# Kernel optimization log

Hardware: AMD Instinct MI355X
Metric: run time of the kernel (lower is better)

## Reference

```python
import jax, jax.numpy as jnp
import numpy as np

D_MODEL = 1024
NUM_HEADS = 16
HEAD_DIM = D_MODEL // NUM_HEADS


def setup_inputs() -> dict:
    key = jax.random.key(0)
    ks = jax.random.split(key, 5)
    scale = 1.0 / np.sqrt(D_MODEL)
    x = jax.random.normal(ks[0], (2, 2048, D_MODEL), dtype=jnp.float32)
    W_qkv = jax.random.normal(ks[1], (D_MODEL, 3 * D_MODEL), dtype=jnp.float32) * scale
    b_qkv = jnp.zeros((3 * D_MODEL,), dtype=jnp.float32)
    W_proj = jax.random.normal(ks[2], (D_MODEL, D_MODEL), dtype=jnp.float32) * scale
    b_proj = jnp.zeros((D_MODEL,), dtype=jnp.float32)
    return {"x": x, "W_qkv": W_qkv, "b_qkv": b_qkv, "W_proj": W_proj, "b_proj": b_proj}


def reference(x, W_qkv, b_qkv, W_proj, b_proj):
    B, S, D = x.shape
    qkv = x @ W_qkv + b_qkv                      # [B,S,3D]
    qkv = qkv.reshape(B, S, 3, NUM_HEADS, HEAD_DIM)
    qkv = jnp.transpose(qkv, (2, 0, 3, 1, 4))    # [3,B,H,S,hd]
    q, k, v = qkv[0], qkv[1], qkv[2]
    scores = jnp.einsum('bhqd,bhkd->bhqk', q, k) / jnp.sqrt(jnp.asarray(HEAD_DIM, x.dtype))
    probs = jax.nn.softmax(scores, axis=-1)
    out = jnp.einsum('bhqk,bhkd->bhqd', probs, v)  # [B,H,S,hd]
    out = jnp.transpose(out, (0, 2, 1, 3)).reshape(B, S, D)
    return out @ W_proj + b_proj
```

## Files before the change

### kernel.cpp

```cpp
#include <hip/hip_runtime.h>
#include <math.h>

#define B_ 2
#define S_ 2048
#define D_ 1024
#define H_ 16
#define HD_ 64

typedef __bf16 bf16x8 __attribute__((ext_vector_type(8)));
typedef __bf16 bf16x4 __attribute__((ext_vector_type(4)));
typedef __bf16 bf16x2 __attribute__((ext_vector_type(2)));
typedef float f32x4 __attribute__((ext_vector_type(4)));
typedef float f32x16 __attribute__((ext_vector_type(16)));
typedef unsigned u32x2 __attribute__((ext_vector_type(2)));

#define GLOAD16(gsrc, ldst) \
  __builtin_amdgcn_global_load_lds((const __attribute__((address_space(1))) void*)(gsrc), \
                                   (__attribute__((address_space(3))) void*)(ldst), 16, 0, 0)

#define QSCALE 0.18033688f

static __device__ __forceinline__ unsigned pack2(float a, float b) {
    bf16x2 v; v[0] = (__bf16)a; v[1] = (__bf16)b;
    return __builtin_bit_cast(unsigned, v);
}

__global__ __launch_bounds__(256) void prep_k(
    const float* __restrict__ x, __bf16* __restrict__ x_bf,
    const float* __restrict__ Wqkv, __bf16* __restrict__ wq_t,
    const float* __restrict__ Wproj, __bf16* __restrict__ wp_t)
{
    __shared__ float t[64][65];
    const int tid = threadIdx.x;
    const int bid = blockIdx.x;

    if (bid < 2048) {
        int i = (bid * 256 + tid) * 8;
        float4 a = *(const float4*)(x + i);
        float4 b = *(const float4*)(x + i + 4);
        bf16x8 v;
        v[0] = (__bf16)a.x; v[1] = (__bf16)a.y; v[2] = (__bf16)a.z; v[3] = (__bf16)a.w;
        v[4] = (__bf16)b.x; v[5] = (__bf16)b.y; v[6] = (__bf16)b.z; v[7] = (__bf16)b.w;
        *(bf16x8*)(x_bf + i) = v;
        return;
    }

    const float* in; __bf16* outp; int K, N, qcols; float qs; int bx, by;
    if (bid < 2816) {
        int tt = bid - 2048; bx = tt % 48; by = tt / 48;
        in = Wqkv; outp = wq_t; K = D_; N = 3 * D_; qcols = D_; qs = QSCALE;
    } else {
        int tt = bid - 2816; bx = tt % 16; by = tt / 16;
        in = Wproj; outp = wp_t; K = D_; N = D_; qcols = 0; qs = 1.0f;
    }
    const int bj = bx * 64;
    const int bi = by * 64;
    #pragma unroll
    for (int it = 0; it < 4; ++it) {
        int idx = (tid + it * 256) * 4;
        int r = idx >> 6, c = idx & 63;
        float4 v = *(const float4*)(in + (size_t)(bi + r) * N + bj + c);
        t[r][c] = v.x; t[r][c+1] = v.y; t[r][c+2] = v.z; t[r][c+3] = v.w;
    }
    __syncthreads();
    int j = tid & 63;
    int i0 = (tid >> 6) * 16;
    float s = (bj + j) < qcols ? qs : 1.0f;
    bf16x8 h0, h1;
    #pragma unroll
    for (int ii = 0; ii < 8; ++ii) h0[ii] = (__bf16)(t[i0 + ii][j] * s);
    #pragma unroll
    for (int ii = 0; ii < 8; ++ii) h1[ii] = (__bf16)(t[i0 + 8 + ii][j] * s);
    size_t o = (size_t)(bj + j) * K + bi + i0;
    *(bf16x8*)(outp + o) = h0; *(bf16x8*)(outp + o + 8) = h1;
}

template<typename OutT>
__global__ __launch_bounds__(256) void gemm_nt_k(
    const __bf16* __restrict__ A, const __bf16* __restrict__ Bt,
    const float* __restrict__ bias, OutT* __restrict__ C,
    int M, int N, int K, int qcols, float qs)
{
    constexpr int TSZ = 128 * 64;
    __shared__ __bf16 sA[TSZ];
    __shared__ __bf16 sB[TSZ];

    const int tid = threadIdx.x, w = tid >> 6, l = tid & 63;
    const int lr = l & 15, lg = l >> 4;
    const int bm = blockIdx.y * 128, bn = blockIdx.x * 128;
    const int wm = w >> 1, wn = w & 1;

    f32x4 acc[4][4] = {};

    for (int k0 = 0; k0 < K; k0 += 64) {
        __syncthreads();
        #pragma unroll
        for (int c = 0; c < 4; ++c) {
            int q = w * 4 + c;
            int r = q * 8 + (l >> 3);
            int sl = ((l & 7) ^ (r & 7)) * 8;
            GLOAD16(A + (size_t)(bm + r) * K + k0 + sl, sA + q * 512);
            GLOAD16(Bt + (size_t)(bn + r) * K + k0 + sl, sB + q * 512);
        }
        __syncthreads();
        #pragma unroll
        for (int kk = 0; kk < 2; ++kk) {
            bf16x8 ah[4], bh[4];
            #pragma unroll
            for (int i = 0; i < 4; ++i) {
                int ra = wm * 64 + i * 16 + lr;
                int sa = ((kk * 4 + lg) ^ (ra & 7)) * 8;
                ah[i] = *(const bf16x8*)(sA + ra * 64 + sa);
                int rb = wn * 64 + i * 16 + lr;
                int sb = ((kk * 4 + lg) ^ (rb & 7)) * 8;
                bh[i] = *(const bf16x8*)(sB + rb * 64 + sb);
            }
            #pragma unroll
            for (int mi = 0; mi < 4; ++mi)
                #pragma unroll
                for (int ni = 0; ni < 4; ++ni)
                    acc[mi][ni] = __builtin_amdgcn_mfma_f32_16x16x32_bf16(ah[mi], bh[ni], acc[mi][ni], 0, 0, 0);
        }
    }

    #pragma unroll
    for (int ni = 0; ni < 4; ++ni) {
        int col = bn + wn * 64 + ni * 16 + lr;
        float bv = bias[col];
        if (col < qcols) bv *= qs;
        #pragma unroll
        for (int mi = 0; mi < 4; ++mi) {
            #pragma unroll
            for (int r = 0; r < 4; ++r) {
                int row = bm + wm * 64 + mi * 16 + lg * 4 + r;
                float v = acc[mi][ni][r] + bv;
                C[(size_t)row * N + col] = (OutT)v;
            }
        }
    }
}

__global__ __launch_bounds__(512) void attn32_k(
    const __bf16* __restrict__ qkv, __bf16* __restrict__ Pout,
    float* __restrict__ Lout)
{
    __shared__ __bf16 Ks[2][2][64 * 64];
    __shared__ __bf16 Vt[2][2][64 * 64];

    const int tid = threadIdx.x, w = tid >> 6, l = tid & 63;
    const int q32 = l & 31, hi = l >> 5;
    const int bid = blockIdx.x;
    const int X = bid >> 5, hb = bid & 31;
    const int qt = X >> 1, kvh = X & 1;
    const int h = hb >> 1, b = hb & 1;
    const int q0 = qt * 256;
    const int kvbase = kvh * 1024;
    const size_t ldq = 3 * D_;
    const __bf16* Qg = qkv + (size_t)b * S_ * ldq + h * HD_;
    const __bf16* Kg = Qg + D_;
    const __bf16* Vg = Qg + 2 * D_;
    const int qg = q0 + w * 32 + q32;

    bf16x8 qf[4];
    #pragma unroll
    for (int ds = 0; ds < 4; ++ds)
        qf[ds] = *(const bf16x8*)(Qg + (size_t)qg * ldq + ds * 16 + hi * 8);

    const int krow = tid >> 3;
    const int ksl  = (tid & 7) ^ (krow & 7);
    const int vk   = tid & 63;
    const int vd0  = (tid >> 6) * 8;
    int voff[8];
    #pragma unroll
    for (int j = 0; j < 8; ++j)
        voff[j] = (vd0 + j) * 128 + (((vk >> 3) ^ j) * 16) + (vk & 7) * 2;

    f32x16 o[2] = {};
    float lsumA = 0.f, lsumB = 0.f;
    bf16x8 vrA, vrB;

    auto stageK = [&](int lt, int set, int t) {
        GLOAD16(Kg + (size_t)(kvbase + lt * 64 + krow) * ldq + ksl * 8,
                &Ks[set][t][w * 512]);
    };
    auto loadV = [&](int lt) {
        return *(const bf16x8*)(Vg + (size_t)(kvbase + lt * 64 + vk) * ldq + vd0);
    };
    auto writeV = [&](int set, int t, const bf16x8& vr) {
        #pragma unroll
        for (int j = 0; j < 8; ++j)
            *(__bf16*)((char*)&Vt[set][t][0] + voff[j]) = vr[j];
    };

    auto smPack = [&](f32x16 sc[2], bf16x8 pa[2][2], float& ls) {
        float sum = 0.f;
        #pragma unroll
        for (int kb = 0; kb < 2; ++kb)
            #pragma unroll
            for (int i = 0; i < 16; ++i) {
                float pv = __builtin_amdgcn_exp2f(sc[kb][i]);
                sc[kb][i] = pv;
                sum += pv;
            }
        ls += sum;
        #pragma unroll
        for (int kb = 0; kb < 2; ++kb)
            #pragma unroll
            for (int tl = 0; tl < 2; ++tl) {
                int base = tl * 8;
                unsigned A0 = pack2(sc[kb][base + 0], sc[kb][base + 1]);
                unsigned A1 = pack2(sc[kb][base + 2], sc[kb][base + 3]);
                unsigned B0 = pack2(sc[kb][base + 4], sc[kb][base + 5]);
                unsigned B1 = pack2(sc[kb][base + 6], sc[kb][base + 7]);
                u32x2 s0 = __builtin_amdgcn_permlane32_swap(A0, B0, false, false);
                u32x2 s1 = __builtin_amdgcn_permlane32_swap(A1, B1, false, false);
                union { unsigned u[4]; bf16x8 v; } pu;
                pu.u[0] = s0[0]; pu.u[1] = s1[0]; pu.u[2] = s0[1]; pu.u[3] = s1[1];
                pa[kb][tl] = pu.v;
            }
    };

    auto computePair = [&](int set) {
        f32x16 sc0[2] = {};
        __builtin_amdgcn_s_setprio(1);
        #pragma unroll
        for (int kb = 0; kb < 2; ++kb) {
            int r = kb * 32 + q32;
            #pragma unroll
            for (int ds = 0; ds < 4; ++ds) {
                int slot = (ds * 2 + hi) ^ (r & 7);
                bf16x8 kf = *(const bf16x8*)((const char*)&Ks[set][0][0] + r * 128 + slot * 16);
                sc0[kb] = __builtin_amdgcn_mfma_f32_32x32x16_bf16(kf, qf[ds], sc0[kb], 0, 0, 0);
            }
        }
        __builtin_amdgcn_s_setprio(0);

        bf16x8 pa0[2][2];
        smPack(sc0, pa0, lsumA);

        f32x16 sc1[2] = {};
        __builtin_amdgcn_s_setprio(1);
        #pragma unroll
        for (int st = 0; st < 4; ++st) {
            {
                int r = q32;
                int slot = (st * 2 + hi) ^ (r & 7);
                bf16x8 kf = *(const bf16x8*)((const char*)&Ks[set][1][0] + r * 128 + slot * 16);
                sc1[0] = __builtin_amdgcn_mfma_f32_32x32x16_bf16(kf, qf[st], sc1[0], 0, 0, 0);
            }
            {
                int dr = q32;
                int slot = (st * 2 + hi) ^ (dr & 7);
                bf16x8 vf = *(const bf16x8*)((const char*)&Vt[set][0][0] + dr * 128 + slot * 16);
                o[0] = __builtin_amdgcn_mfma_f32_32x32x16_bf16(vf, pa0[st >> 1][st & 1], o[0], 0, 0, 0);
            }
            {
                int r = 32 + q32;
                int slot = (st * 2 + hi) ^ (r & 7);
                bf16x8 kf = *(const bf16x8*)((const char*)&Ks[set][1][0] + r * 128 + slot * 16);
                sc1[1] = __builtin_amdgcn_mfma_f32_32x32x16_bf16(kf, qf[st], sc1[1], 0, 0, 0);
            }
            {
                int dr = 32 + q32;
                int slot = (st * 2 + hi) ^ (dr & 7);
                bf16x8 vf = *(const bf16x8*)((const char*)&Vt[set][0][0] + dr * 128 + slot * 16);
                o[1] = __builtin_amdgcn_mfma_f32_32x32x16_bf16(vf, pa0[st >> 1][st & 1], o[1], 0, 0, 0);
            }
        }
        __builtin_amdgcn_s_setprio(0);

        bf16x8 pa1[2][2];
        smPack(sc1, pa1, lsumB);

        __builtin_amdgcn_s_setprio(1);
        #pragma unroll
        for (int db = 0; db < 2; ++db) {
            int dr = db * 32 + q32;
            #pragma unroll
            for (int tt = 0; tt < 4; ++tt) {
                int slot = (tt * 2 + hi) ^ (dr & 7);
                bf16x8 vf = *(const bf16x8*)((const char*)&Vt[set][1][0] + dr * 128 + slot * 16);
                o[db] = __builtin_amdgcn_mfma_f32_32x32x16_bf16(vf, pa1[tt >> 1][tt & 1], o[db], 0, 0, 0);
            }
        }
        __builtin_amdgcn_s_setprio(0);
    };

    stageK(0, 0, 0); stageK(1, 0, 1);
    vrA = loadV(0);  vrB = loadV(1);
    writeV(0, 0, vrA); writeV(0, 1, vrB);
    __syncthreads();

    constexpr int NP = 8;
    for (int pr = 0; pr < NP; ++pr) {
        const int set = pr & 1, nset = set ^ 1;
        if (pr < NP - 1) {
            stageK(2 * pr + 2, nset, 0);
            stageK(2 * pr + 3, nset, 1);
            vrA = loadV(2 * pr + 2);
            vrB = loadV(2 * pr + 3);
        }
        computePair(set);
        if (pr < NP - 1) {
            writeV(nset, 0, vrA);
            writeV(nset, 1, vrB);
        }
        __syncthreads();
    }

    float lsum = lsumA + lsumB;
    lsum += __shfl_xor(lsum, 32);
    const size_t orow = (size_t)b * S_ + qg;
    __bf16* Pb = Pout + (size_t)kvh * (4096 * 1024) + orow * D_ + h * HD_;
    #pragma unroll
    for (int db = 0; db < 2; ++db)
        #pragma unroll
        for (int rg = 0; rg < 4; ++rg) {
            int d = db * 32 + 8 * rg + 4 * hi;
            bf16x4 ov;
            #pragma unroll
            for (int i = 0; i < 4; ++i) ov[i] = (__bf16)o[db][rg * 4 + i];
            *(bf16x4*)(Pb + d) = ov;
        }
    if (hi == 0)
        Lout[(size_t)kvh * (4096 * 16) + orow * 16 + h] = lsum;
}

__global__ __launch_bounds__(256) void combine_k(
    const __bf16* __restrict__ P, const float* __restrict__ L,
    __bf16* __restrict__ attnb)
{
    int i = (blockIdx.x * 256 + threadIdx.x) * 8;
    int row = i >> 10;
    int h = (i & 1023) >> 6;
    float l0 = L[row * 16 + h];
    float l1 = L[4096 * 16 + row * 16 + h];
    float inv = 1.0f / (l0 + l1);
    bf16x8 p0 = *(const bf16x8*)(P + i);
    bf16x8 p1 = *(const bf16x8*)(P + 4096 * 1024 + i);
    bf16x8 r;
    #pragma unroll
    for (int j = 0; j < 8; ++j)
        r[j] = (__bf16)(((float)p0[j] + (float)p1[j]) * inv);
    *(bf16x8*)(attnb + i) = r;
}

extern "C" void kernel_launch(void* const* d_in, const int* in_sizes, int n_in,
                              void* d_out, int out_size, void* d_ws, size_t ws_size,
                              hipStream_t stream) {
    const float* x     = (const float*)d_in[0];
    const float* Wqkv  = (const float*)d_in[1];
    const float* bqkv  = (const float*)d_in[2];
    const float* Wproj = (const float*)d_in[3];
    const float* bproj = (const float*)d_in[4];

    __bf16* ws = (__bf16*)d_ws;
    const size_t MB = 524288;
    __bf16* wp_t  = ws;
    __bf16* qkv   = ws + 2 * MB;
    __bf16* attnb = ws + 26 * MB;
    __bf16* x_bf  = ws + 34 * MB;
    __bf16* wq_t  = ws + 42 * MB;
    __bf16* Pp    = ws + 34 * MB;
    float*  Lp    = (float*)(ws + 50 * MB);

    const int M = B_ * S_;

    prep_k<<<3072, 256, 0, stream>>>(x, x_bf, Wqkv, wq_t, Wproj, wp_t);

    gemm_nt_k<__bf16><<<dim3(24, 32), 256, 0, stream>>>(
        x_bf, wq_t, bqkv, qkv, M, 3 * D_, D_, D_, QSCALE);

    attn32_k<<<512, 512, 0, stream>>>(qkv, Pp, Lp);

    combine_k<<<2048, 256, 0, stream>>>(Pp, Lp, attnb);

    gemm_nt_k<float><<<dim3(8, 32), 256, 0, stream>>>(
        attnb, wp_t, bproj, (float*)d_out, M, D_, D_, 0, 1.0f);
}
```

Measured before the change: 136.3 us.

## Restructure attention to 4 waves each owning 64 queries, sharing K/V fragments

The attention kernel now runs 4 waves of 256 threads instead of 8, and each wave handles two 32-query groups. Every K and V fragment read from LDS feeds two MFMAs, which halves the LDS reads per unit of math. The K/V tiles shrink to one 64-row tile per stage, double-buffered, and the loop runs over 16 single tiles instead of 8 pairs. This gives up the interleaved pair schedule, which overlapped QK^T of the second tile with PV of the first, and it roughly doubles accumulator and Q register use per wave, which could limit occupancy. Launch bounds ask for 2 blocks per CU.

```diff
diff --git a/kernel.cpp b/kernel.cpp
--- a/kernel.cpp
+++ b/kernel.cpp
@@ -140,12 +140,12 @@
     }
 }
 
-__global__ __launch_bounds__(512) void attn32_k(
+__global__ __launch_bounds__(256, 2) void attn32_k(
     const __bf16* __restrict__ qkv, __bf16* __restrict__ Pout,
     float* __restrict__ Lout)
 {
-    __shared__ __bf16 Ks[2][2][64 * 64];
-    __shared__ __bf16 Vt[2][2][64 * 64];
+    __shared__ __bf16 Ks[2][64 * 64];
+    __shared__ __bf16 Vt[2][64 * 64];
 
     const int tid = threadIdx.x, w = tid >> 6, l = tid & 63;
     const int q32 = l & 31, hi = l >> 5;
@@ -159,37 +159,49 @@
     const __bf16* Qg = qkv + (size_t)b * S_ * ldq + h * HD_;
     const __bf16* Kg = Qg + D_;
     const __bf16* Vg = Qg + 2 * D_;
-    const int qg = q0 + w * 32 + q32;
-
-    bf16x8 qf[4];
-    #pragma unroll
-    for (int ds = 0; ds < 4; ++ds)
-        qf[ds] = *(const bf16x8*)(Qg + (size_t)qg * ldq + ds * 16 + hi * 8);
-
-    const int krow = tid >> 3;
-    const int ksl  = (tid & 7) ^ (krow & 7);
-    const int vk   = tid & 63;
-    const int vd0  = (tid >> 6) * 8;
-    int voff[8];
-    #pragma unroll
-    for (int j = 0; j < 8; ++j)
-        voff[j] = (vd0 + j) * 128 + (((vk >> 3) ^ j) * 16) + (vk & 7) * 2;
-
-    f32x16 o[2] = {};
-    float lsumA = 0.f, lsumB = 0.f;
-    bf16x8 vrA, vrB;
-
-    auto stageK = [&](int lt, int set, int t) {
-        GLOAD16(Kg + (size_t)(kvbase + lt * 64 + krow) * ldq + ksl * 8,
-                &Ks[set][t][w * 512]);
+    const int qg0 = q0 + w * 64 + q32;
+
+    bf16x8 qf0[4], qf1[4];
+    #pragma unroll
+    for (int ds = 0; ds < 4; ++ds) {
+        qf0[ds] = *(const bf16x8*)(Qg + (size_t)qg0 * ldq + ds * 16 + hi * 8);
+        qf1[ds] = *(const bf16x8*)(Qg + (size_t)(qg0 + 32) * ldq + ds * 16 + hi * 8);
+    }
+
+    int krow[2], ksl[2], voff[2][8];
+    const int vk = l;
+    #pragma unroll
+    for (int c = 0; c < 2; ++c) {
+        int p = (w * 2 + c) * 64 + l;
+        krow[c] = p >> 3;
+        ksl[c]  = (p & 7) ^ (krow[c] & 7);
+        int d0 = (w * 2 + c) * 8;
+        #pragma unroll
+        for (int j = 0; j < 8; ++j)
+            voff[c][j] = (d0 + j) * 128 + (((vk >> 3) ^ j) * 16) + (vk & 7) * 2;
+    }
+
+    f32x16 o0[2] = {}, o1[2] = {};
+    float lsum0 = 0.f, lsum1 = 0.f;
+    bf16x8 vr[2];
+
+    auto stageK = [&](int lt, int buf) {
+        #pragma unroll
+        for (int c = 0; c < 2; ++c)
+            GLOAD16(Kg + (size_t)(kvbase + lt * 64 + krow[c]) * ldq + ksl[c] * 8,
+                    &Ks[buf][(w * 2 + c) * 512]);
     };
     auto loadV = [&](int lt) {
-        return *(const bf16x8*)(Vg + (size_t)(kvbase + lt * 64 + vk) * ldq + vd0);
-    };
-    auto writeV = [&](int set, int t, const bf16x8& vr) {
-        #pragma unroll
-        for (int j = 0; j < 8; ++j)
-            *(__bf16*)((char*)&Vt[set][t][0] + voff[j]) = vr[j];
+        #pragma unroll
+        for (int c = 0; c < 2; ++c)
+            vr[c] = *(const bf16x8*)(Vg + (size_t)(kvbase + lt * 64 + vk) * ldq + (w * 2 + c) * 8);
+    };
+    auto writeV = [&](int buf) {
+        #pragma unroll
+        for (int c = 0; c < 2; ++c)
+            #pragma unroll
+            for (int j = 0; j < 8; ++j)
+                *(__bf16*)((char*)&Vt[buf][0] + voff[c][j]) = vr[c][j];
     };
 
     auto smPack = [&](f32x16 sc[2], bf16x8 pa[2][2], float& ls) {
@@ -220,8 +232,8 @@
             }
     };
 
-    auto computePair = [&](int set) {
-        f32x16 sc0[2] = {};
+    auto computeTile = [&](int cur) {
+        f32x16 sc0[2] = {}, sc1[2] = {};
         __builtin_amdgcn_s_setprio(1);
         #pragma unroll
         for (int kb = 0; kb < 2; ++kb) {
@@ -229,48 +241,16 @@
             #pragma unroll
             for (int ds = 0; ds < 4; ++ds) {
                 int slot = (ds * 2 + hi) ^ (r & 7);
-                bf16x8 kf = *(const bf16x8*)((const char*)&Ks[set][0][0] + r * 128 + slot * 16);
-                sc0[kb] = __builtin_amdgcn_mfma_f32_32x32x16_bf16(kf, qf[ds], sc0[kb], 0, 0, 0);
+                bf16x8 kf = *(const bf16x8*)((const char*)&Ks[cur][0] + r * 128 + slot * 16);
+                sc0[kb] = __builtin_amdgcn_mfma_f32_32x32x16_bf16(kf, qf0[ds], sc0[kb], 0, 0, 0);
+                sc1[kb] = __builtin_amdgcn_mfma_f32_32x32x16_bf16(kf, qf1[ds], sc1[kb], 0, 0, 0);
             }
         }
         __builtin_amdgcn_s_setprio(0);
 
-        bf16x8 pa0[2][2];
-        smPack(sc0, pa0, lsumA);
-
-        f32x16 sc1[2] = {};
-        __builtin_amdgcn_s_setprio(1);
-        #pragma unroll
-        for (int st = 0; st < 4; ++st) {
-            {
-                int r = q32;
-                int slot = (st * 2 + hi) ^ (r & 7);
-                bf16x8 kf = *(const bf16x8*)((const char*)&Ks[set][1][0] + r * 128 + slot * 16);
-                sc1[0] = __builtin_amdgcn_mfma_f32_32x32x16_bf16(kf, qf[st], sc1[0], 0, 0, 0);
-            }
-            {
-                int dr = q32;
-                int slot = (st * 2 + hi) ^ (dr & 7);
-                bf16x8 vf = *(const bf16x8*)((const char*)&Vt[set][0][0] + dr * 128 + slot * 16);
-                o[0] = __builtin_amdgcn_mfma_f32_32x32x16_bf16(vf, pa0[st >> 1][st & 1], o[0], 0, 0, 0);
-            }
-            {
-                int r = 32 + q32;
-                int slot = (st * 2 + hi) ^ (r & 7);
-                bf16x8 kf = *(const bf16x8*)((const char*)&Ks[set][1][0] + r * 128 + slot * 16);
-                sc1[1] = __builtin_amdgcn_mfma_f32_32x32x16_bf16(kf, qf[st], sc1[1], 0, 0, 0);
-            }
-            {
-                int dr = 32 + q32;
-                int slot = (st * 2 + hi) ^ (dr & 7);
-                bf16x8 vf = *(const bf16x8*)((const char*)&Vt[set][0][0] + dr * 128 + slot * 16);
-                o[1] = __builtin_amdgcn_mfma_f32_32x32x16_bf16(vf, pa0[st >> 1][st & 1], o[1], 0, 0, 0);
-            }
-        }
-        __builtin_amdgcn_s_setprio(0);
-
-        bf16x8 pa1[2][2];
-        smPack(sc1, pa1, lsumB);
+        bf16x8 pa0[2][2], pa1[2][2];
+        smPack(sc0, pa0, lsum0);
+        smPack(sc1, pa1, lsum1);
 
         __builtin_amdgcn_s_setprio(1);
         #pragma unroll
@@ -279,51 +259,51 @@
             #pragma unroll
             for (int tt = 0; tt < 4; ++tt) {
                 int slot = (tt * 2 + hi) ^ (dr & 7);
-                bf16x8 vf = *(const bf16x8*)((const char*)&Vt[set][1][0] + dr * 128 + slot * 16);
-                o[db] = __builtin_amdgcn_mfma_f32_32x32x16_bf16(vf, pa1[tt >> 1][tt & 1], o[db], 0, 0, 0);
+                bf16x8 vf = *(const bf16x8*)((const char*)&Vt[cur][0] + dr * 128 + slot * 16);
+                o0[db] = __builtin_amdgcn_mfma_f32_32x32x16_bf16(vf, pa0[tt >> 1][tt & 1], o0[db], 0, 0, 0);
+                o1[db] = __builtin_amdgcn_mfma_f32_32x32x16_bf16(vf, pa1[tt >> 1][tt & 1], o1[db], 0, 0, 0);
             }
         }
         __builtin_amdgcn_s_setprio(0);
     };
 
-    stageK(0, 0, 0); stageK(1, 0, 1);
-    vrA = loadV(0);  vrB = loadV(1);
-    writeV(0, 0, vrA); writeV(0, 1, vrB);
+    stageK(0, 0);
+    loadV(0);
+    writeV(0);
     __syncthreads();
 
-    constexpr int NP = 8;
-    for (int pr = 0; pr < NP; ++pr) {
-        const int set = pr & 1, nset = set ^ 1;
-        if (pr < NP - 1) {
-            stageK(2 * pr + 2, nset, 0);
-            stageK(2 * pr + 3, nset, 1);
-            vrA = loadV(2 * pr + 2);
-            vrB = loadV(2 * pr + 3);
-        }
-        computePair(set);
-        if (pr < NP - 1) {
-            writeV(nset, 0, vrA);
-            writeV(nset, 1, vrB);
-        }
+    constexpr int NT = 16;
+    for (int kt = 0; kt < NT; ++kt) {
+        const int cur = kt & 1, nxt = cur ^ 1;
+        if (kt < NT - 1) { stageK(kt + 1, nxt); loadV(kt + 1); }
+        computeTile(cur);
+        if (kt < NT - 1) writeV(nxt);
         __syncthreads();
     }
 
-    float lsum = lsumA + lsumB;
-    lsum += __shfl_xor(lsum, 32);
-    const size_t orow = (size_t)b * S_ + qg;
-    __bf16* Pb = Pout + (size_t)kvh * (4096 * 1024) + orow * D_ + h * HD_;
+    lsum0 += __shfl_xor(lsum0, 32);
+    lsum1 += __shfl_xor(lsum1, 32);
+    const size_t orow0 = (size_t)b * S_ + qg0;
+    __bf16* Pb0 = Pout + (size_t)kvh * (4096 * 1024) + orow0 * D_ + h * HD_;
+    __bf16* Pb1 = Pb0 + (size_t)32 * D_;
     #pragma unroll
     for (int db = 0; db < 2; ++db)
         #pragma unroll
         for (int rg = 0; rg < 4; ++rg) {
             int d = db * 32 + 8 * rg + 4 * hi;
-            bf16x4 ov;
-            #pragma unroll
-            for (int i = 0; i < 4; ++i) ov[i] = (__bf16)o[db][rg * 4 + i];
-            *(bf16x4*)(Pb + d) = ov;
-        }
-    if (hi == 0)
-        Lout[(size_t)kvh * (4096 * 16) + orow * 16 + h] = lsum;
+            bf16x4 ov0, ov1;
+            #pragma unroll
+            for (int i = 0; i < 4; ++i) {
+                ov0[i] = (__bf16)o0[db][rg * 4 + i];
+                ov1[i] = (__bf16)o1[db][rg * 4 + i];
+            }
+            *(bf16x4*)(Pb0 + d) = ov0;
+            *(bf16x4*)(Pb1 + d) = ov1;
+        }
+    if (hi == 0) {
+        Lout[(size_t)kvh * (4096 * 16) + orow0 * 16 + h] = lsum0;
+        Lout[(size_t)kvh * (4096 * 16) + (orow0 + 32) * 16 + h] = lsum1;
+    }
 }
 
 __global__ __launch_bounds__(256) void combine_k(
@@ -371,7 +351,7 @@
     gemm_nt_k<__bf16><<<dim3(24, 32), 256, 0, stream>>>(
         x_bf, wq_t, bqkv, qkv, M, 3 * D_, D_, D_, QSCALE);
 
-    attn32_k<<<512, 512, 0, stream>>>(qkv, Pp, Lp);
+    attn32_k<<<512, 256, 0, stream>>>(qkv, Pp, Lp);
 
     combine_k<<<2048, 256, 0, stream>>>(Pp, Lp, attnb);
 
```

After: 129.7 us. 1.05x faster.
